# Optimization experiments

Hardware: AMD Instinct MI355X
Metric: run time of the kernel (lower is better)

The kernel has to match this reference:

```python
import jax, jax.numpy as jnp
import numpy as np
import math

B, C, P, D, R = 64, 32, 256, 128, 32
HID = max(D // 4, 8)  # adaptive-gate hidden = 32
GIN = 2 * D + 1       # adaptive-gate input dim = 257


def setup_inputs() -> dict:
    key = jax.random.key(0)
    ks = jax.random.split(key, 16)
    s = 0.05
    return {
        "x": jax.random.normal(ks[0], (B * C, P, D), dtype=jnp.float32),
        "gamma": jnp.ones((D,), jnp.float32),
        "beta": jnp.zeros((D,), jnp.float32),
        "W_down": jax.random.normal(ks[1], (D, R), jnp.float32) * s,
        "b_down": jax.random.normal(ks[2], (R,), jnp.float32) * s,
        "W_q": jax.random.normal(ks[3], (R, R), jnp.float32) * s,
        "W_k": jax.random.normal(ks[4], (R, R), jnp.float32) * s,
        "W_v": jax.random.normal(ks[5], (R, R), jnp.float32) * s,
        "W_cg": jax.random.normal(ks[6], (R, R), jnp.float32) * s,
        "b_cg": jax.random.normal(ks[7], (R,), jnp.float32) * s,
        "W_up": jax.random.normal(ks[8], (R, D), jnp.float32) * s,
        "b_up": jax.random.normal(ks[9], (D,), jnp.float32) * s,
        "Wg1": jax.random.normal(ks[10], (GIN, HID), jnp.float32) * s,
        "bg1": jax.random.normal(ks[11], (HID,), jnp.float32) * s,
        "Wg2": jax.random.normal(ks[12], (HID, D), jnp.float32) * s,
        "bg2": jnp.full((D,), -5.0, jnp.float32) + jax.random.normal(ks[13], (D,), jnp.float32) * s,
        "B": B,
        "C": C,
    }


def _l2norm(t, eps=1e-12):
    n = jnp.sqrt(jnp.sum(t * t, axis=-1, keepdims=True))
    return t / jnp.maximum(n, eps)


def _layernorm(h, gamma, beta, eps=1e-5):
    mu = jnp.mean(h, axis=-1, keepdims=True)
    var = jnp.mean(jnp.square(h - mu), axis=-1, keepdims=True)
    return (h - mu) * jax.lax.rsqrt(var + eps) * gamma + beta


def reference(x, gamma, beta, W_down, b_down, W_q, W_k, W_v, W_cg, b_cg,
              W_up, b_up, Wg1, bg1, Wg2, bg2, B, C):
    BC, Pn, Dn = x.shape
    # [B*C,P,D] -> [B*P,C,D]
    h = x.reshape(B, C, Pn, Dn).transpose(0, 2, 1, 3).reshape(B * Pn, C, Dn)
    h_norm = _layernorm(h, gamma, beta)
    # bottleneck projection
    h_low = h_norm @ W_down + b_down          # [BP, C, R]
    # Hydra linear attention (cosine similarity)
    Q = _l2norm(h_low @ W_q)                  # [BP, C, R]
    K = _l2norm(h_low @ W_k)
    V = h_low @ W_v
    global_feat = jnp.sum(K * V, axis=1, keepdims=True)  # [BP, 1, R]
    h_attn = Q * global_feat                  # [BP, C, R]
    # content gate + up-projection
    cg = jax.nn.sigmoid(h_low @ W_cg + b_cg)
    mixed = (h_attn * cg) @ W_up + b_up       # [BP, C, D]
    # adaptive channel-aware gate
    chan_var = jnp.var(h, axis=1, ddof=1)     # [BP, D] (torch unbiased var)
    chan_mean_abs = jnp.mean(jnp.abs(h), axis=1)  # [BP, D]
    log_c = jnp.full((h.shape[0], 1), math.log(max(C, 2)) / math.log(1000),
                     dtype=h.dtype)
    gate_in = jnp.concatenate([chan_var, chan_mean_abs, log_c], axis=1)
    g1 = jax.nn.gelu(gate_in @ Wg1 + bg1, approximate=False)
    gate = jax.nn.sigmoid(g1 @ Wg2 + bg2)[:, None, :]  # [BP, 1, D]
    out = h + gate * mixed                    # [BP, C, D]
    # back to [B*C, P, D]
    return out.reshape(B, Pn, C, Dn).transpose(0, 2, 1, 3).reshape(BC, Pn, Dn)
```

## Files before the change

### kernel.cpp

```cpp
#include <hip/hip_runtime.h>

typedef unsigned short u16t;
typedef unsigned int   u32t;

__device__ __forceinline__ float bf2f(u16t u) {
  union { u32t i; float f; } v; v.i = ((u32t)u) << 16; return v.f;
}
__device__ __forceinline__ u32t f2bf_bits(float f) {
  union { float f; u32t u; } v; v.f = f;
  u32t u = v.u;
  u += 0x7fffu + ((u >> 16) & 1u);
  return u >> 16;
}
__device__ __forceinline__ float sigmoidf_(float x) { return 1.f / (1.f + expf(-x)); }
__device__ __forceinline__ float bflo(u32t w) {
  union { u32t i; float f; } v; v.i = w << 16; return v.f;
}
__device__ __forceinline__ float bfhi(u32t w) {
  union { u32t i; float f; } v; v.i = w & 0xffff0000u; return v.f;
}

template <bool BF> __device__ __forceinline__ float gld(const void* p, int i) {
  if constexpr (BF) return bf2f(((const u16t*)p)[i]);
  else return ((const float*)p)[i];
}
template <bool BF> __device__ __forceinline__ void gld4(const void* p, int i, float* o) {
  if constexpr (BF) {
    ushort4 w = *(const ushort4*)((const u16t*)p + i);
    o[0] = bf2f(w.x); o[1] = bf2f(w.y); o[2] = bf2f(w.z); o[3] = bf2f(w.w);
  } else {
    float4 w = *(const float4*)((const float*)p + i);
    o[0] = w.x; o[1] = w.y; o[2] = w.z; o[3] = w.w;
  }
}
__device__ __forceinline__ void unpack8(uint4 w, float* o) {
  u32t a[4] = {w.x, w.y, w.z, w.w};
#pragma unroll
  for (int j = 0; j < 4; ++j) { o[2 * j] = bflo(a[j]); o[2 * j + 1] = bfhi(a[j]); }
}
__device__ __forceinline__ void gld8bf(const void* p, long long i, float* o) {
  unpack8(*(const uint4*)((const u16t*)p + i), o);
}
__device__ __forceinline__ u32t packbf(float a, float b) {
  return f2bf_bits(a) | (f2bf_bits(b) << 16);
}

template <bool BF>
__device__ __forceinline__ void fillw(u16t* dst, const void* src, int nelem, int t) {
  const int nch = nelem >> 3;
  for (int k = t; k < nch; k += 256) {
    if constexpr (BF) {
      *(uint4*)(dst + (k << 3)) = *(const uint4*)((const u16t*)src + (k << 3));
    } else {
      const float* s = (const float*)src + (k << 3);
      float4 a = *(const float4*)s;
      float4 b = *(const float4*)(s + 4);
      *(uint4*)(dst + (k << 3)) =
          make_uint4(packbf(a.x, a.y), packbf(a.z, a.w),
                     packbf(b.x, b.y), packbf(b.z, b.w));
    }
  }
}

template <bool BF>
__global__ __launch_bounds__(256, 4) void hydra_kernel(
    const void* __restrict__ x,
    const void* __restrict__ g_gamma, const void* __restrict__ g_beta,
    const void* __restrict__ Wd,  const void* __restrict__ bd,
    const void* __restrict__ Wq,  const void* __restrict__ Wk,
    const void* __restrict__ Wv,  const void* __restrict__ Wcg,
    const void* __restrict__ bcg, const void* __restrict__ Wup,
    const void* __restrict__ bup, const void* __restrict__ Wg1,
    const void* __restrict__ bg1, const void* __restrict__ Wg2,
    const void* __restrict__ bg2, void* __restrict__ out)
{
  {
    u32t w0 = *(const u32t*)g_gamma;
    bool gamma_is_bf16 = (w0 == 0x3F803F80u);
    if (gamma_is_bf16 != BF) return;
  }

  __shared__ alignas(16) u16t  sh_w[12288];
  __shared__ alignas(16) u16t  sh_hs[32 * 136];
  __shared__ alignas(16) u16t  sh_hn[32 * 136];
  __shared__ alignas(16) float sh_hlow[32 * 33];
  __shared__ alignas(16) float sh_stat[768];
  __shared__ float sh_gin[257];
  __shared__ alignas(16) float sh_gfp[128];
  __shared__ float sh_g1[32];
  __shared__ alignas(16) float sh_gate[128];

  const int u  = threadIdx.x;
  const int bp = blockIdx.x;
  const int b  = bp >> 8;
  const int p  = bp & 255;
  const int c  = u >> 3;
  const int q  = u & 7;
  const long long rowe = ((long long)((b * 32 + c) * 256 + p)) * 128;

  float hreg[16];
  if constexpr (BF) {
    const u16t* xp = (const u16t*)x + rowe;
    uint4 w0 = *(const uint4*)(xp + q * 8);
    uint4 w1 = *(const uint4*)(xp + 64 + q * 8);
    *(uint4*)&sh_hs[c * 136 + q * 8]      = w0;
    *(uint4*)&sh_hs[c * 136 + 64 + q * 8] = w1;
    unpack8(w0, hreg);
    unpack8(w1, hreg + 8);
  } else {
    const float* xp = (const float*)x + rowe;
#pragma unroll
    for (int ch = 0; ch < 4; ++ch) {
      float4 w = *(const float4*)(xp + ch * 32 + q * 4);
      hreg[ch * 4 + 0] = w.x; hreg[ch * 4 + 1] = w.y;
      hreg[ch * 4 + 2] = w.z; hreg[ch * 4 + 3] = w.w;
      *(uint2*)&sh_hs[c * 136 + ch * 32 + q * 4] =
          make_uint2(packbf(w.x, w.y), packbf(w.z, w.w));
    }
  }
  fillw<BF>(sh_w + 0,    Wd,  4096, u);
  fillw<BF>(sh_w + 4096, Wq,  1024, u);
  fillw<BF>(sh_w + 5120, Wk,  1024, u);
  fillw<BF>(sh_w + 6144, Wv,  1024, u);
  fillw<BF>(sh_w + 7168, Wcg, 1024, u);
  fillw<BF>(sh_w + 8192, Wup, 4096, u);

  float s = 0.f, ss = 0.f;
#pragma unroll
  for (int i = 0; i < 16; ++i) { s += hreg[i]; ss += hreg[i] * hreg[i]; }
#pragma unroll
  for (int m = 1; m < 8; m <<= 1) {
    s  += __shfl_xor(s,  m);
    ss += __shfl_xor(ss, m);
  }
  const float mu   = s * (1.f / 128.f);
  const float var  = ss * (1.f / 128.f) - mu * mu;
  const float rstd = rsqrtf(var + 1e-5f);
  if constexpr (BF) {
#pragma unroll
    for (int half = 0; half < 2; ++half) {
      const int d0 = half * 64 + q * 8;
      float ga[8], be[8];
      gld8bf(g_gamma, d0, ga);
      gld8bf(g_beta,  d0, be);
      u32t pk[4];
#pragma unroll
      for (int j = 0; j < 4; ++j) {
        float f0 = (hreg[half * 8 + 2 * j]     - mu) * rstd * ga[2 * j]     + be[2 * j];
        float f1 = (hreg[half * 8 + 2 * j + 1] - mu) * rstd * ga[2 * j + 1] + be[2 * j + 1];
        pk[j] = packbf(f0, f1);
      }
      *(uint4*)&sh_hn[c * 136 + d0] = make_uint4(pk[0], pk[1], pk[2], pk[3]);
    }
  } else {
#pragma unroll
    for (int ch = 0; ch < 4; ++ch) {
      const int d0 = ch * 32 + q * 4;
      float ga[4], be[4];
      gld4<false>(g_gamma, d0, ga);
      gld4<false>(g_beta,  d0, be);
      float f0 = (hreg[ch * 4 + 0] - mu) * rstd * ga[0] + be[0];
      float f1 = (hreg[ch * 4 + 1] - mu) * rstd * ga[1] + be[1];
      float f2 = (hreg[ch * 4 + 2] - mu) * rstd * ga[2] + be[2];
      float f3 = (hreg[ch * 4 + 3] - mu) * rstd * ga[3] + be[3];
      *(uint2*)&sh_hn[c * 136 + d0] = make_uint2(packbf(f0, f1), packbf(f2, f3));
    }
  }
  __syncthreads();

  {
    const int d = u & 127, half = u >> 7;
    float s1 = 0.f, s2 = 0.f, s3 = 0.f;
#pragma unroll
    for (int ci = 0; ci < 16; ++ci) {
      float v = bf2f(sh_hs[(half * 16 + ci) * 136 + d]);
      s1 += v; s2 += v * v; s3 += fabsf(v);
    }
    sh_stat[half * 384 +   0 + d] = s1;
    sh_stat[half * 384 + 128 + d] = s2;
    sh_stat[half * 384 + 256 + d] = s3;
  }
  {
    const int r0 = q * 4;
    float bi[4];
    gld4<BF>(bd, r0, bi);
    float a0 = bi[0], a1 = bi[1], a2 = bi[2], a3 = bi[3];
    const u32t* hnp = (const u32t*)sh_hn + c * 68;
    const u32t* w32 = (const u32t*)sh_w;
#pragma unroll 4
    for (int d2 = 0; d2 < 64; ++d2) {
      u32t hp = hnp[d2];
      float h0 = bflo(hp), h1 = bfhi(hp);
      uint2 wa = *(const uint2*)(w32 + d2 * 32 + q * 2);
      uint2 wb = *(const uint2*)(w32 + d2 * 32 + 16 + q * 2);
      a0 += h0 * bflo(wa.x); a1 += h0 * bfhi(wa.x);
      a2 += h0 * bflo(wa.y); a3 += h0 * bfhi(wa.y);
      a0 += h1 * bflo(wb.x); a1 += h1 * bfhi(wb.x);
      a2 += h1 * bflo(wb.y); a3 += h1 * bfhi(wb.y);
    }
    sh_hlow[c * 33 + r0 + 0] = a0;
    sh_hlow[c * 33 + r0 + 1] = a1;
    sh_hlow[c * 33 + r0 + 2] = a2;
    sh_hlow[c * 33 + r0 + 3] = a3;
  }
  __syncthreads();

  if (u < 128) {
    const int d = u;
    float S  = sh_stat[d]       + sh_stat[384 + d];
    float SS = sh_stat[128 + d] + sh_stat[384 + 128 + d];
    float SA = sh_stat[256 + d] + sh_stat[384 + 256 + d];
    sh_gin[d]       = (SS - S * S * (1.f / 32.f)) * (1.f / 31.f);
    sh_gin[128 + d] = SA * (1.f / 32.f);
    if (u == 0) sh_gin[256] = 0.501716659439968f;
  }
  float qn0, qn1, qn2, qn3, cg0, cg1, cg2, cg3;
  {
    const int r0 = q * 4;
    float aq0 = 0, aq1 = 0, aq2 = 0, aq3 = 0;
    float ak0 = 0, ak1 = 0, ak2 = 0, ak3 = 0;
    float av0 = 0, av1 = 0, av2 = 0, av3 = 0;
    float ac0 = 0, ac1 = 0, ac2 = 0, ac3 = 0;
    const u32t* w32 = (const u32t*)sh_w;
#pragma unroll 2
    for (int k = 0; k < 32; ++k) {
      float hl = sh_hlow[c * 33 + k];
      uint2 w2;
      w2 = *(const uint2*)(w32 + 2048 + k * 16 + q * 2);
      aq0 += hl * bflo(w2.x); aq1 += hl * bfhi(w2.x);
      aq2 += hl * bflo(w2.y); aq3 += hl * bfhi(w2.y);
      w2 = *(const uint2*)(w32 + 2560 + k * 16 + q * 2);
      ak0 += hl * bflo(w2.x); ak1 += hl * bfhi(w2.x);
      ak2 += hl * bflo(w2.y); ak3 += hl * bfhi(w2.y);
      w2 = *(const uint2*)(w32 + 3072 + k * 16 + q * 2);
      av0 += hl * bflo(w2.x); av1 += hl * bfhi(w2.x);
      av2 += hl * bflo(w2.y); av3 += hl * bfhi(w2.y);
      w2 = *(const uint2*)(w32 + 3584 + k * 16 + q * 2);
      ac0 += hl * bflo(w2.x); ac1 += hl * bfhi(w2.x);
      ac2 += hl * bflo(w2.y); ac3 += hl * bfhi(w2.y);
    }
    float qss = aq0 * aq0 + aq1 * aq1 + aq2 * aq2 + aq3 * aq3;
    float kss = ak0 * ak0 + ak1 * ak1 + ak2 * ak2 + ak3 * ak3;
#pragma unroll
    for (int m = 1; m < 8; m <<= 1) {
      qss += __shfl_xor(qss, m);
      kss += __shfl_xor(kss, m);
    }
    float qinv = 1.f / fmaxf(sqrtf(qss), 1e-12f);
    float kinv = 1.f / fmaxf(sqrtf(kss), 1e-12f);
    float kv0 = (ak0 * kinv) * av0;
    float kv1 = (ak1 * kinv) * av1;
    float kv2 = (ak2 * kinv) * av2;
    float kv3 = (ak3 * kinv) * av3;
#pragma unroll
    for (int m = 8; m < 64; m <<= 1) {
      kv0 += __shfl_xor(kv0, m);
      kv1 += __shfl_xor(kv1, m);
      kv2 += __shfl_xor(kv2, m);
      kv3 += __shfl_xor(kv3, m);
    }
    if ((u & 63) < 8) {
      float* gp = &sh_gfp[(u >> 6) * 32 + r0];
      gp[0] = kv0; gp[1] = kv1; gp[2] = kv2; gp[3] = kv3;
    }
    qn0 = aq0 * qinv; qn1 = aq1 * qinv; qn2 = aq2 * qinv; qn3 = aq3 * qinv;
    float bb[4];
    gld4<BF>(bcg, r0, bb);
    cg0 = sigmoidf_(ac0 + bb[0]);
    cg1 = sigmoidf_(ac1 + bb[1]);
    cg2 = sigmoidf_(ac2 + bb[2]);
    cg3 = sigmoidf_(ac3 + bb[3]);
  }
  __syncthreads();

  {
    const int j = u & 31, ig = u >> 5;
    const int i0 = ig * 32;
    const int cnt = (ig == 7) ? 33 : 32;
    float acc = 0.f;
    for (int t2 = 0; t2 < cnt; ++t2)
      acc += sh_gin[i0 + t2] * gld<BF>(Wg1, (i0 + t2) * 32 + j);
    sh_stat[ig * 32 + j] = acc;
  }
  __syncthreads();

  if (u < 32) {
    float z = gld<BF>(bg1, u);
#pragma unroll
    for (int ch = 0; ch < 8; ++ch) z += sh_stat[ch * 32 + u];
    sh_g1[u] = 0.5f * z * (1.f + erff(z * 0.7071067811865475f));
  }
  {
    const int r0 = q * 4;
    float4 g0 = *(const float4*)&sh_gfp[r0];
    float4 g1v = *(const float4*)&sh_gfp[32 + r0];
    float4 g2 = *(const float4*)&sh_gfp[64 + r0];
    float4 g3 = *(const float4*)&sh_gfp[96 + r0];
    float* ap = sh_hlow;
    ap[c * 33 + r0 + 0] = qn0 * (g0.x + g1v.x + g2.x + g3.x) * cg0;
    ap[c * 33 + r0 + 1] = qn1 * (g0.y + g1v.y + g2.y + g3.y) * cg1;
    ap[c * 33 + r0 + 2] = qn2 * (g0.z + g1v.z + g2.z + g3.z) * cg2;
    ap[c * 33 + r0 + 3] = qn3 * (g0.w + g1v.w + g2.w + g3.w) * cg3;
  }
  __syncthreads();

  if (u < 128) {
    float acc = gld<BF>(bg2, u);
#pragma unroll 4
    for (int k = 0; k < 32; ++k) acc += sh_g1[k] * gld<BF>(Wg2, k * 128 + u);
    sh_gate[u] = sigmoidf_(acc);
  }
  float acc[16];
  {
    if constexpr (BF) {
      gld8bf(bup, q * 8,      acc);
      gld8bf(bup, 64 + q * 8, acc + 8);
    } else {
#pragma unroll
      for (int ch = 0; ch < 4; ++ch) gld4<false>(bup, ch * 32 + q * 4, acc + ch * 4);
    }
    const float* ap = sh_hlow;
    const u32t* w32 = (const u32t*)sh_w;
#pragma unroll 2
    for (int k = 0; k < 32; ++k) {
      float av = ap[c * 33 + k];
      if constexpr (BF) {
        uint4 wA = *(const uint4*)(w32 + 4096 + k * 64 + q * 4);
        uint4 wB = *(const uint4*)(w32 + 4096 + k * 64 + 32 + q * 4);
        acc[0]  += av * bflo(wA.x); acc[1]  += av * bfhi(wA.x);
        acc[2]  += av * bflo(wA.y); acc[3]  += av * bfhi(wA.y);
        acc[4]  += av * bflo(wA.z); acc[5]  += av * bfhi(wA.z);
        acc[6]  += av * bflo(wA.w); acc[7]  += av * bfhi(wA.w);
        acc[8]  += av * bflo(wB.x); acc[9]  += av * bfhi(wB.x);
        acc[10] += av * bflo(wB.y); acc[11] += av * bfhi(wB.y);
        acc[12] += av * bflo(wB.z); acc[13] += av * bfhi(wB.z);
        acc[14] += av * bflo(wB.w); acc[15] += av * bfhi(wB.w);
      } else {
#pragma unroll
        for (int ch = 0; ch < 4; ++ch) {
          uint2 w2 = *(const uint2*)(w32 + 4096 + k * 64 + ch * 16 + q * 2);
          acc[ch * 4 + 0] += av * bflo(w2.x);
          acc[ch * 4 + 1] += av * bfhi(w2.x);
          acc[ch * 4 + 2] += av * bflo(w2.y);
          acc[ch * 4 + 3] += av * bfhi(w2.y);
        }
      }
    }
  }
  __syncthreads();
  if constexpr (BF) {
    float gt[16];
    {
      float4 g;
      g = *(const float4*)&sh_gate[q * 8];          gt[0]=g.x; gt[1]=g.y; gt[2]=g.z; gt[3]=g.w;
      g = *(const float4*)&sh_gate[q * 8 + 4];      gt[4]=g.x; gt[5]=g.y; gt[6]=g.z; gt[7]=g.w;
      g = *(const float4*)&sh_gate[64 + q * 8];     gt[8]=g.x; gt[9]=g.y; gt[10]=g.z; gt[11]=g.w;
      g = *(const float4*)&sh_gate[64 + q * 8 + 4]; gt[12]=g.x; gt[13]=g.y; gt[14]=g.z; gt[15]=g.w;
    }
    u32t ov[8];
#pragma unroll
    for (int j = 0; j < 8; ++j) {
      float o0 = hreg[2 * j]     + gt[2 * j]     * acc[2 * j];
      float o1 = hreg[2 * j + 1] + gt[2 * j + 1] * acc[2 * j + 1];
      ov[j] = packbf(o0, o1);
    }
    u16t* ob = (u16t*)out + rowe;
    *(uint4*)(ob + q * 8)      = make_uint4(ov[0], ov[1], ov[2], ov[3]);
    *(uint4*)(ob + 64 + q * 8) = make_uint4(ov[4], ov[5], ov[6], ov[7]);
  } else {
    float* op = (float*)out + rowe;
#pragma unroll
    for (int ch = 0; ch < 4; ++ch) {
      float4 g4 = *(const float4*)&sh_gate[ch * 32 + q * 4];
      float4 o4;
      o4.x = hreg[ch * 4 + 0] + g4.x * acc[ch * 4 + 0];
      o4.y = hreg[ch * 4 + 1] + g4.y * acc[ch * 4 + 1];
      o4.z = hreg[ch * 4 + 2] + g4.z * acc[ch * 4 + 2];
      o4.w = hreg[ch * 4 + 3] + g4.w * acc[ch * 4 + 3];
      *(float4*)(op + ch * 32 + q * 4) = o4;
    }
  }
}

extern "C" void kernel_launch(void* const* d_in, const int* in_sizes, int n_in,
                              void* d_out, int out_size, void* d_ws, size_t ws_size,
                              hipStream_t stream) {
  const int FP32_BYTES = 1 << 28;
  const int BF16_BYTES = 1 << 27;
  const int sz = (in_sizes != nullptr) ? in_sizes[0] : 0;
  const bool launch_f32 = (sz != BF16_BYTES);
  const bool launch_bf  = (sz != FP32_BYTES);
  if (launch_bf)
    hydra_kernel<true><<<dim3(64 * 256), dim3(256), 0, stream>>>(
        d_in[0],  d_in[1],  d_in[2],  d_in[3],  d_in[4],  d_in[5],
        d_in[6],  d_in[7],  d_in[8],  d_in[9],  d_in[10], d_in[11],
        d_in[12], d_in[13], d_in[14], d_in[15], d_out);
  if (launch_f32)
    hydra_kernel<false><<<dim3(64 * 256), dim3(256), 0, stream>>>(
        d_in[0],  d_in[1],  d_in[2],  d_in[3],  d_in[4],  d_in[5],
        d_in[6],  d_in[7],  d_in[8],  d_in[9],  d_in[10], d_in[11],
        d_in[12], d_in[13], d_in[14], d_in[15], d_out);
}
```

Before: 777.5 us.

## Use v_dot2_f32_bf16 with k-pair-packed weight layout in shared memory

Weights are repacked in shared memory so that consecutive k rows are interleaved into a single 32-bit word per output column. The projections (down, q/k/v/cg, up) then use the v_dot2_f32_bf16 instruction, which handles two k-terms per op. Intermediate activations (h_low, the attention product) are stored as packed bf16 pairs instead of fp32, which halves the shared memory they use and the ALU work in the inner loops. In exchange, the weight fill now does strided scalar global loads, and h_low and the mixed activations lose precision from the extra rounding to bf16.

```diff
diff --git a/kernel.cpp b/kernel.cpp
--- a/kernel.cpp
+++ b/kernel.cpp
@@ -18,6 +18,11 @@
 }
 __device__ __forceinline__ float bfhi(u32t w) {
   union { u32t i; float f; } v; v.i = w & 0xffff0000u; return v.f;
+}
+__device__ __forceinline__ float dot2bf(u32t a, u32t b, float c) {
+  float d;
+  asm("v_dot2_f32_bf16 %0, %1, %2, %3" : "=v"(d) : "v"(a), "v"(b), "v"(c));
+  return d;
 }
 
 template <bool BF> __device__ __forceinline__ float gld(const void* p, int i) {
@@ -45,20 +50,22 @@
   return f2bf_bits(a) | (f2bf_bits(b) << 16);
 }
 
-template <bool BF>
-__device__ __forceinline__ void fillw(u16t* dst, const void* src, int nelem, int t) {
-  const int nch = nelem >> 3;
-  for (int k = t; k < nch; k += 256) {
+template <bool BF, int LOG2C>
+__device__ __forceinline__ void fillw_pk(u32t* dst, const void* src, int total, int t) {
+  for (int o = t; o < total; o += 256) {
+    const int k2 = o >> LOG2C;
+    const int r  = o & ((1 << LOG2C) - 1);
+    const int i0 = (k2 << (LOG2C + 1)) + r;
+    const int i1 = i0 + (1 << LOG2C);
+    u32t w;
     if constexpr (BF) {
-      *(uint4*)(dst + (k << 3)) = *(const uint4*)((const u16t*)src + (k << 3));
+      u32t lo = ((const u16t*)src)[i0];
+      u32t hi = ((const u16t*)src)[i1];
+      w = lo | (hi << 16);
     } else {
-      const float* s = (const float*)src + (k << 3);
-      float4 a = *(const float4*)s;
-      float4 b = *(const float4*)(s + 4);
-      *(uint4*)(dst + (k << 3)) =
-          make_uint4(packbf(a.x, a.y), packbf(a.z, a.w),
-                     packbf(b.x, b.y), packbf(b.z, b.w));
-    }
+      w = packbf(((const float*)src)[i0], ((const float*)src)[i1]);
+    }
+    dst[o] = w;
   }
 }
 
@@ -80,10 +87,16 @@
     if (gamma_is_bf16 != BF) return;
   }
 
-  __shared__ alignas(16) u16t  sh_w[12288];
-  __shared__ alignas(16) u16t  sh_hs[32 * 136];
-  __shared__ alignas(16) u16t  sh_hn[32 * 136];
-  __shared__ alignas(16) float sh_hlow[32 * 33];
+  __shared__ alignas(16) u32t sh_wd [64 * 32];
+  __shared__ alignas(16) u32t sh_wq [16 * 32];
+  __shared__ alignas(16) u32t sh_wk [16 * 32];
+  __shared__ alignas(16) u32t sh_wv [16 * 32];
+  __shared__ alignas(16) u32t sh_wcg[16 * 32];
+  __shared__ alignas(16) u32t sh_wup[16 * 128];
+  __shared__ alignas(16) u16t sh_hs[32 * 136];
+  __shared__ alignas(16) u16t sh_hn[32 * 136];
+  __shared__ alignas(16) u32t sh_hlow[32 * 18];
+  __shared__ alignas(16) u32t sh_apk [32 * 18];
   __shared__ alignas(16) float sh_stat[768];
   __shared__ float sh_gin[257];
   __shared__ alignas(16) float sh_gfp[128];
@@ -118,12 +131,12 @@
           make_uint2(packbf(w.x, w.y), packbf(w.z, w.w));
     }
   }
-  fillw<BF>(sh_w + 0,    Wd,  4096, u);
-  fillw<BF>(sh_w + 4096, Wq,  1024, u);
-  fillw<BF>(sh_w + 5120, Wk,  1024, u);
-  fillw<BF>(sh_w + 6144, Wv,  1024, u);
-  fillw<BF>(sh_w + 7168, Wcg, 1024, u);
-  fillw<BF>(sh_w + 8192, Wup, 4096, u);
+  fillw_pk<BF, 5>(sh_wd,  Wd,  2048, u);
+  fillw_pk<BF, 5>(sh_wq,  Wq,  512,  u);
+  fillw_pk<BF, 5>(sh_wk,  Wk,  512,  u);
+  fillw_pk<BF, 5>(sh_wv,  Wv,  512,  u);
+  fillw_pk<BF, 5>(sh_wcg, Wcg, 512,  u);
+  fillw_pk<BF, 7>(sh_wup, Wup, 2048, u);
 
   float s = 0.f, ss = 0.f;
 #pragma unroll
@@ -186,22 +199,16 @@
     gld4<BF>(bd, r0, bi);
     float a0 = bi[0], a1 = bi[1], a2 = bi[2], a3 = bi[3];
     const u32t* hnp = (const u32t*)sh_hn + c * 68;
-    const u32t* w32 = (const u32t*)sh_w;
-#pragma unroll 4
+#pragma unroll 8
     for (int d2 = 0; d2 < 64; ++d2) {
       u32t hp = hnp[d2];
-      float h0 = bflo(hp), h1 = bfhi(hp);
-      uint2 wa = *(const uint2*)(w32 + d2 * 32 + q * 2);
-      uint2 wb = *(const uint2*)(w32 + d2 * 32 + 16 + q * 2);
-      a0 += h0 * bflo(wa.x); a1 += h0 * bfhi(wa.x);
-      a2 += h0 * bflo(wa.y); a3 += h0 * bfhi(wa.y);
-      a0 += h1 * bflo(wb.x); a1 += h1 * bfhi(wb.x);
-      a2 += h1 * bflo(wb.y); a3 += h1 * bfhi(wb.y);
-    }
-    sh_hlow[c * 33 + r0 + 0] = a0;
-    sh_hlow[c * 33 + r0 + 1] = a1;
-    sh_hlow[c * 33 + r0 + 2] = a2;
-    sh_hlow[c * 33 + r0 + 3] = a3;
+      uint4 w = *(const uint4*)(sh_wd + d2 * 32 + r0);
+      a0 = dot2bf(hp, w.x, a0);
+      a1 = dot2bf(hp, w.y, a1);
+      a2 = dot2bf(hp, w.z, a2);
+      a3 = dot2bf(hp, w.w, a3);
+    }
+    *(uint2*)&sh_hlow[c * 18 + q * 2] = make_uint2(packbf(a0, a1), packbf(a2, a3));
   }
   __syncthreads();
 
@@ -221,23 +228,22 @@
     float ak0 = 0, ak1 = 0, ak2 = 0, ak3 = 0;
     float av0 = 0, av1 = 0, av2 = 0, av3 = 0;
     float ac0 = 0, ac1 = 0, ac2 = 0, ac3 = 0;
-    const u32t* w32 = (const u32t*)sh_w;
-#pragma unroll 2
-    for (int k = 0; k < 32; ++k) {
-      float hl = sh_hlow[c * 33 + k];
-      uint2 w2;
-      w2 = *(const uint2*)(w32 + 2048 + k * 16 + q * 2);
-      aq0 += hl * bflo(w2.x); aq1 += hl * bfhi(w2.x);
-      aq2 += hl * bflo(w2.y); aq3 += hl * bfhi(w2.y);
-      w2 = *(const uint2*)(w32 + 2560 + k * 16 + q * 2);
-      ak0 += hl * bflo(w2.x); ak1 += hl * bfhi(w2.x);
-      ak2 += hl * bflo(w2.y); ak3 += hl * bfhi(w2.y);
-      w2 = *(const uint2*)(w32 + 3072 + k * 16 + q * 2);
-      av0 += hl * bflo(w2.x); av1 += hl * bfhi(w2.x);
-      av2 += hl * bflo(w2.y); av3 += hl * bfhi(w2.y);
-      w2 = *(const uint2*)(w32 + 3584 + k * 16 + q * 2);
-      ac0 += hl * bflo(w2.x); ac1 += hl * bfhi(w2.x);
-      ac2 += hl * bflo(w2.y); ac3 += hl * bfhi(w2.y);
+#pragma unroll 4
+    for (int k2 = 0; k2 < 16; ++k2) {
+      u32t hp = sh_hlow[c * 18 + k2];
+      uint4 w;
+      w = *(const uint4*)(sh_wq + k2 * 32 + r0);
+      aq0 = dot2bf(hp, w.x, aq0); aq1 = dot2bf(hp, w.y, aq1);
+      aq2 = dot2bf(hp, w.z, aq2); aq3 = dot2bf(hp, w.w, aq3);
+      w = *(const uint4*)(sh_wk + k2 * 32 + r0);
+      ak0 = dot2bf(hp, w.x, ak0); ak1 = dot2bf(hp, w.y, ak1);
+      ak2 = dot2bf(hp, w.z, ak2); ak3 = dot2bf(hp, w.w, ak3);
+      w = *(const uint4*)(sh_wv + k2 * 32 + r0);
+      av0 = dot2bf(hp, w.x, av0); av1 = dot2bf(hp, w.y, av1);
+      av2 = dot2bf(hp, w.z, av2); av3 = dot2bf(hp, w.w, av3);
+      w = *(const uint4*)(sh_wcg + k2 * 32 + r0);
+      ac0 = dot2bf(hp, w.x, ac0); ac1 = dot2bf(hp, w.y, ac1);
+      ac2 = dot2bf(hp, w.z, ac2); ac3 = dot2bf(hp, w.w, ac3);
     }
     float qss = aq0 * aq0 + aq1 * aq1 + aq2 * aq2 + aq3 * aq3;
     float kss = ak0 * ak0 + ak1 * ak1 + ak2 * ak2 + ak3 * ak3;
@@ -296,11 +302,11 @@
     float4 g1v = *(const float4*)&sh_gfp[32 + r0];
     float4 g2 = *(const float4*)&sh_gfp[64 + r0];
     float4 g3 = *(const float4*)&sh_gfp[96 + r0];
-    float* ap = sh_hlow;
-    ap[c * 33 + r0 + 0] = qn0 * (g0.x + g1v.x + g2.x + g3.x) * cg0;
-    ap[c * 33 + r0 + 1] = qn1 * (g0.y + g1v.y + g2.y + g3.y) * cg1;
-    ap[c * 33 + r0 + 2] = qn2 * (g0.z + g1v.z + g2.z + g3.z) * cg2;
-    ap[c * 33 + r0 + 3] = qn3 * (g0.w + g1v.w + g2.w + g3.w) * cg3;
+    float a0 = qn0 * (g0.x + g1v.x + g2.x + g3.x) * cg0;
+    float a1 = qn1 * (g0.y + g1v.y + g2.y + g3.y) * cg1;
+    float a2 = qn2 * (g0.z + g1v.z + g2.z + g3.z) * cg2;
+    float a3 = qn3 * (g0.w + g1v.w + g2.w + g3.w) * cg3;
+    *(uint2*)&sh_apk[c * 18 + q * 2] = make_uint2(packbf(a0, a1), packbf(a2, a3));
   }
   __syncthreads();
 
@@ -319,30 +325,30 @@
 #pragma unroll
       for (int ch = 0; ch < 4; ++ch) gld4<false>(bup, ch * 32 + q * 4, acc + ch * 4);
     }
-    const float* ap = sh_hlow;
-    const u32t* w32 = (const u32t*)sh_w;
-#pragma unroll 2
-    for (int k = 0; k < 32; ++k) {
-      float av = ap[c * 33 + k];
+#pragma unroll 4
+    for (int k2 = 0; k2 < 16; ++k2) {
+      u32t ap = sh_apk[c * 18 + k2];
       if constexpr (BF) {
-        uint4 wA = *(const uint4*)(w32 + 4096 + k * 64 + q * 4);
-        uint4 wB = *(const uint4*)(w32 + 4096 + k * 64 + 32 + q * 4);
-        acc[0]  += av * bflo(wA.x); acc[1]  += av * bfhi(wA.x);
-        acc[2]  += av * bflo(wA.y); acc[3]  += av * bfhi(wA.y);
-        acc[4]  += av * bflo(wA.z); acc[5]  += av * bfhi(wA.z);
-        acc[6]  += av * bflo(wA.w); acc[7]  += av * bfhi(wA.w);
-        acc[8]  += av * bflo(wB.x); acc[9]  += av * bfhi(wB.x);
-        acc[10] += av * bflo(wB.y); acc[11] += av * bfhi(wB.y);
-        acc[12] += av * bflo(wB.z); acc[13] += av * bfhi(wB.z);
-        acc[14] += av * bflo(wB.w); acc[15] += av * bfhi(wB.w);
+        uint4 wA = *(const uint4*)(sh_wup + k2 * 128 + q * 8);
+        uint4 wB = *(const uint4*)(sh_wup + k2 * 128 + q * 8 + 4);
+        uint4 wC = *(const uint4*)(sh_wup + k2 * 128 + 64 + q * 8);
+        uint4 wD = *(const uint4*)(sh_wup + k2 * 128 + 64 + q * 8 + 4);
+        acc[0]  = dot2bf(ap, wA.x, acc[0]);  acc[1]  = dot2bf(ap, wA.y, acc[1]);
+        acc[2]  = dot2bf(ap, wA.z, acc[2]);  acc[3]  = dot2bf(ap, wA.w, acc[3]);
+        acc[4]  = dot2bf(ap, wB.x, acc[4]);  acc[5]  = dot2bf(ap, wB.y, acc[5]);
+        acc[6]  = dot2bf(ap, wB.z, acc[6]);  acc[7]  = dot2bf(ap, wB.w, acc[7]);
+        acc[8]  = dot2bf(ap, wC.x, acc[8]);  acc[9]  = dot2bf(ap, wC.y, acc[9]);
+        acc[10] = dot2bf(ap, wC.z, acc[10]); acc[11] = dot2bf(ap, wC.w, acc[11]);
+        acc[12] = dot2bf(ap, wD.x, acc[12]); acc[13] = dot2bf(ap, wD.y, acc[13]);
+        acc[14] = dot2bf(ap, wD.z, acc[14]); acc[15] = dot2bf(ap, wD.w, acc[15]);
       } else {
 #pragma unroll
         for (int ch = 0; ch < 4; ++ch) {
-          uint2 w2 = *(const uint2*)(w32 + 4096 + k * 64 + ch * 16 + q * 2);
-          acc[ch * 4 + 0] += av * bflo(w2.x);
-          acc[ch * 4 + 1] += av * bfhi(w2.x);
-          acc[ch * 4 + 2] += av * bflo(w2.y);
-          acc[ch * 4 + 3] += av * bfhi(w2.y);
+          uint4 w = *(const uint4*)(sh_wup + k2 * 128 + ch * 32 + q * 4);
+          acc[ch * 4 + 0] = dot2bf(ap, w.x, acc[ch * 4 + 0]);
+          acc[ch * 4 + 1] = dot2bf(ap, w.y, acc[ch * 4 + 1]);
+          acc[ch * 4 + 2] = dot2bf(ap, w.z, acc[ch * 4 + 2]);
+          acc[ch * 4 + 3] = dot2bf(ap, w.w, acc[ch * 4 + 3]);
         }
       }
     }
```

After: 678.0 us. 12.8% less time.
